# Kernel tuning notes

Hardware: AMD Instinct MI355X
Metric: run time of the kernel (lower is better)

Reference implementation:

```python
import jax, jax.numpy as jnp
import numpy as np

EPS = 1e-30
NEG = -1e30  # finite stand-in for -inf (safe under vjp, exp underflows to 0)


def _build_tree(L):
    """Perfect binary tree with L leaves (L power of 2) plus a unifurcating root.
    Node ids are level-contiguous (leaves first), which is a valid postorder-compatible
    numbering for the level-synchronous pruning loop."""
    depth = int(np.log2(L))
    total = 2 * L  # (2L-1) perfect-tree nodes + 1 unifurcating root
    children = np.full((total, 2), -1, dtype=np.int64)
    parents = np.full(total, -1, dtype=np.int64)
    levels = np.zeros(total, dtype=np.int64)
    offs = np.zeros(depth + 1, dtype=np.int64)
    for h in range(1, depth + 1):
        offs[h] = offs[h - 1] + (L >> (h - 1))
    for h in range(1, depth + 1):
        n = L >> h
        ids = offs[h] + np.arange(n)
        lkid = offs[h - 1] + 2 * np.arange(n)
        children[ids, 0] = lkid
        children[ids, 1] = lkid + 1
        parents[lkid] = ids
        parents[lkid + 1] = ids
        levels[ids] = h
    root = total - 1
    top = offs[depth]  # the single node at level `depth`
    children[root, 0] = top  # unifurcating root: right child = -1
    parents[top] = root
    levels[root] = depth + 1
    return children, parents, levels


def setup_inputs() -> dict:
    key = jax.random.key(0)
    S = 16
    L = 32768  # leaves -> N = 65536 nodes
    children, parents, levels = _build_tree(L)
    N = children.shape[0]
    postorder = np.arange(N, dtype=np.int64)
    k1, k2, k3, k4 = jax.random.split(key, 4)
    branch_lens = jax.random.uniform(k1, (N,), jnp.float32, 0.05, 0.5)
    branch_lens = branch_lens.at[N - 1].set(0.0)  # root edge has length 0
    # CTMC-style rate matrix: nonneg off-diagonals, rows sum to 0
    off = jax.random.uniform(k2, (S, S), jnp.float32, 0.1, 1.0) * (1.0 - jnp.eye(S, dtype=jnp.float32))
    Q = off - jnp.diag(off.sum(axis=1))
    growth_rates = jax.random.uniform(k3, (S,), jnp.float32, 0.5, 1.5)
    leaf_states = np.asarray(jax.random.randint(k4, (L,), 0, S))
    init_partials = np.full((N, S), NEG, dtype=np.float32)
    init_partials[np.arange(L), leaf_states] = 0.0  # leaf one-hots in log space
    return {
        "postorder": jnp.asarray(postorder),
        "children": jnp.asarray(children),
        "parents": jnp.asarray(parents),
        "branch_lens": branch_lens,
        "init_partials": jnp.asarray(init_partials),
        "Q": Q,
        "levels": jnp.asarray(levels),
        "growth_rates": growth_rates,
    }


def _log_prune(branch_lens, init_partials, Q, growth_rates, po, ch, lv):
    S = Q.shape[0]
    # rho == 1.0 path of FelsensteinPruner.log_prune
    rate = Q - jnp.diag(growth_rates)
    scaled = rate[None, :, :] * branch_lens[:, None, None]      # (N, S, S)
    trans = jax.vmap(jax.scipy.linalg.expm)(scaled)             # batched matrix_exp
    I = jnp.eye(S, dtype=Q.dtype)
    trans = jnp.where((branch_lens <= EPS)[:, None, None], I[None], trans)
    log_trans = jnp.log(jnp.clip(trans, EPS))
    log_growth = jnp.log(growth_rates)
    log_partials = init_partials
    max_level = int(lv.max())
    for lvl in range(1, max_level + 1):  # tree topology is static -> static level groups
        node_idxs = po[lv == lvl]
        left = ch[node_idxs, 0]
        right = ch[node_idxs, 1]
        # left_contrib[n, p] = logsumexp_c( log P_left[n, p, c] + L_left[n, c] )
        lc = jax.nn.logsumexp(log_trans[left] + log_partials[left][:, None, :], axis=2)
        valid = np.nonzero(right >= 0)[0]
        rc = jnp.zeros_like(lc)
        if valid.size > 0:
            rv = right[valid]
            rc_v = jax.nn.logsumexp(log_trans[rv] + log_partials[rv][:, None, :], axis=2)
            rc_v = rc_v + log_growth[None, :]  # growth_rates term on the right child
            rc = rc.at[valid].set(rc_v)
        log_partials = log_partials.at[node_idxs].set(lc + rc)
    root = int(po[lv == max_level][0])
    return log_partials[root]


def reference(postorder, children, parents, branch_lens, init_partials, Q, levels, growth_rates):
    po = np.asarray(postorder)
    ch = np.asarray(children)
    lv = np.asarray(levels)
    return _log_prune(branch_lens, init_partials, Q, growth_rates, po, ch, lv)
```

## Files before the change

kernel.cpp:

```cpp
#include <hip/hip_runtime.h>
#include <math.h>

#define KORD 10
#define NC   (KORD + 1)
#define NTOT 65536
#define MAGIC 0x5A17C0DEu
#define NB   256
#define CB0  240

typedef float f32x2 __attribute__((ext_vector_type(2)));

static constexpr int WS_U7  = 0;
static constexpr int WS_S7  = 4096;
static constexpr int WS_U11 = 4352;
static constexpr int WS_S11 = 4608;
static constexpr int WS_F1  = 4624;
static constexpr int WS_F2  = 4880;


template <int CTRL>
__device__ __forceinline__ float qperm_add(float x) {
  const int xi = __builtin_bit_cast(int, x);
  const int yi = __builtin_amdgcn_mov_dpp(xi, CTRL, 0xF, 0xF, true);
  return x + __builtin_bit_cast(float, yi);
}

__device__ __forceinline__ float horner_dot(const f32x2* c01, const f32x2* c23,
                                            float tv, float4 uu) {
  const f32x2 t2 = {tv, tv};
  f32x2 a01 = c01[KORD], a23 = c23[KORD];
  #pragma unroll
  for (int k = KORD - 1; k >= 0; --k) {
    a01 = __builtin_elementwise_fma(a01, t2, c01[k]);
    a23 = __builtin_elementwise_fma(a23, t2, c23[k]);
  }
  const f32x2 u01 = {uu.x, uu.y}, u23 = {uu.z, uu.w};
  f32x2 mm = a01 * u01;
  mm = __builtin_elementwise_fma(a23, u23, mm);
  float yy = mm.x + mm.y;
  yy = qperm_add<0xB1>(yy);
  yy = qperm_add<0x4E>(yy);
  return yy;
}

__device__ __forceinline__ int tree_sweep(
    float* ubuf, float* sbuf, const float* blB,
    const f32x2* c01, const f32x2* c23, float sigma, float gp,
    int IN, int depth, int t)
{
  const int lane = t & 63;
  const int wid = t >> 6;
  const int p = (lane >> 2) & 15;
  const int q = lane & 3;
  int off_in = 0, bloff = 0;
  for (int ll = 1; ll <= depth; ++ll) {
    const int cnt = IN >> ll;
    const int off_out = off_in + (IN >> (ll - 1));
    for (int n = wid; n < cnt; n += 8) {
      const int cl = 2 * n, cr = cl + 1;
      const float tl = blB[bloff + cl];
      const float tr = blB[bloff + cr];
      const float4 uL = *(const float4*)&ubuf[(off_in + cl) * 16 + q * 4];
      const float4 uR = *(const float4*)&ubuf[(off_in + cr) * 16 + q * 4];
      const float yl = horner_dot(c01, c23, tl, uL);
      const float yr = horner_dot(c01, c23, tr, uR);
      const float val = yl * yr * gp;
      const float mx = __shfl(val, 28 + q, 64);
      const float un = val * __builtin_amdgcn_rcpf(mx);
      if (q == 0) ubuf[(off_out + n) * 16 + p] = un;
      if (lane == 0)
        sbuf[off_out + n] = sbuf[off_in + cl] + sbuf[off_in + cr] +
                            sigma * (tl + tr) + __logf(mx);
    }
    bloff += IN >> (ll - 1);
    off_in = off_out;
    __syncthreads();
  }
  return off_in;
}

__device__ __forceinline__ void stage_bl(float* blB, const float* bl,
                                         int grp, int IN, int depth,
                                         int level_in, int tt) {
  int loff = 0;
  for (int ll = 1; ll <= depth; ++ll) {
    const int cnt_c = IN >> (ll - 1);
    const int gl = level_in + ll - 1;
    const int cbase = (gl == 0) ? 0 : (NTOT - (NTOT >> gl));
    if (tt < cnt_c) blB[loff + tt] = bl[cbase + grp * cnt_c + tt];
    loff += cnt_c;
  }
}

__device__ __forceinline__ void poll_reset(unsigned int* f) {
  while (__hip_atomic_load(f, __ATOMIC_RELAXED, __HIP_MEMORY_SCOPE_AGENT)
         != MAGIC)
    __builtin_amdgcn_s_sleep(1);
  __hip_atomic_store(f, 0u, __ATOMIC_RELAXED, __HIP_MEMORY_SCOPE_AGENT);
}

__device__ __forceinline__ float row_dot16(const float4* row, const float* col) {
  const float4 r0 = row[0], r1 = row[1], r2 = row[2], r3 = row[3];
  float s = r0.x * col[0];
  s = fmaf(r0.y, col[1], s);  s = fmaf(r0.z, col[2], s);
  s = fmaf(r0.w, col[3], s);  s = fmaf(r1.x, col[4], s);
  s = fmaf(r1.y, col[5], s);  s = fmaf(r1.z, col[6], s);
  s = fmaf(r1.w, col[7], s);  s = fmaf(r2.x, col[8], s);
  s = fmaf(r2.y, col[9], s);  s = fmaf(r2.z, col[10], s);
  s = fmaf(r2.w, col[11], s); s = fmaf(r3.x, col[12], s);
  s = fmaf(r3.y, col[13], s); s = fmaf(r3.z, col[14], s);
  s = fmaf(r3.w, col[15], s);
  return s;
}

__global__ __launch_bounds__(512) void k_all(
    const float* __restrict__ bl, const float* __restrict__ init_p,
    const float* __restrict__ Q, const float* __restrict__ g,
    float* __restrict__ ws, float* __restrict__ out)
{
  __shared__ __align__(16) float Bs[256];
  __shared__ __align__(16) float BsT[256];
  __shared__ __align__(16) float B2T[256];
  __shared__ __align__(16) float Cs[NC * 256];
  __shared__ __align__(16) float ubuf[255 * 16];
  __shared__ float sbuf[255];
  __shared__ float blB[254];
  __shared__ float sdiag[16];
  __shared__ float s_sig;

  const int t = threadIdx.x, b = blockIdx.x;
  const int lane = t & 63, wid = t >> 6;
  const int p = (lane >> 2) & 15, q = lane & 3;
  const int i = (t & 255) >> 4, j = t & 15;
  const int tt = t - 256;
  unsigned int* f1 = (unsigned int*)(ws + WS_F1);
  unsigned int* f2 = (unsigned int*)(ws + WS_F2);

  float4 leafv = ((const float4*)init_p)[b * 512 + t];
  float blr[7];
  if (t >= 256) {
    int cnt = 128, base = 0;
    #pragma unroll
    for (int ll = 1; ll <= 7; ++ll) {
      if (tt < cnt) blr[ll - 1] = bl[base + b * cnt + tt];
      base = NTOT - (NTOT >> ll);
      cnt >>= 1;
    }
  }

  float a = 0.0f;
  if (t < 256) {
    a = Q[t] - ((i == j) ? g[i] : 0.0f);
    if (i == j) sdiag[i] = a;
  }
  __syncthreads();
  if (t == 0) {
    float m = sdiag[0];
    for (int r = 1; r < 16; ++r) m = fminf(m, sdiag[r]);
    s_sig = m;
  }
  __syncthreads();
  const float sigma = s_sig;
  if (t < 256) {
    const float bv = a - ((i == j) ? sigma : 0.0f);
    Bs[t] = bv;
    BsT[j * 16 + i] = bv;
    Cs[t] = (i == j) ? 1.0f : 0.0f;
    Cs[256 + t] = bv;
  }
  __syncthreads();
  if (t < 256) {
    float bcol[16];
    #pragma unroll
    for (int c = 0; c < 4; ++c)
      *(float4*)&bcol[c * 4] = *(const float4*)&BsT[j * 16 + c * 4];
    const float s = row_dot16((const float4*)&Bs[i * 16], bcol);
    B2T[j * 16 + i] = s;
  }
  __syncthreads();
  float b2col[16];
  #pragma unroll
  for (int c = 0; c < 4; ++c)
    *(float4*)&b2col[c * 4] = *(const float4*)&B2T[j * 16 + c * 4];
  #pragma unroll
  for (int m = 0; m < 5; ++m) {
    if (t < 256) {
      const float s = row_dot16((const float4*)&Cs[(2 * m) * 256 + i * 16], b2col);
      Cs[(2 * m + 2) * 256 + t] = s * (1.0f / (float)((2 * m + 1) * (2 * m + 2)));
    } else if (m < 4) {
      const float s = row_dot16((const float4*)&Cs[(2 * m + 1) * 256 + i * 16], b2col);
      Cs[(2 * m + 3) * 256 + tt] =
          s * (1.0f / (float)((2 * m + 2) * (2 * m + 3)));
    }
    __syncthreads();
  }
  f32x2 c01[NC], c23[NC];
  #pragma unroll
  for (int k = 0; k <= KORD; ++k) {
    const float4 v = *(const float4*)&Cs[k * 256 + p * 16 + q * 4];
    c01[k] = f32x2{v.x, v.y};
    c23[k] = f32x2{v.z, v.w};
  }
  const float gp = g[p];

  {
    float4 v = leafv;
    v.x = (v.x > -0.5f) ? 1.0f : 0.0f;
    v.y = (v.y > -0.5f) ? 1.0f : 0.0f;
    v.z = (v.z > -0.5f) ? 1.0f : 0.0f;
    v.w = (v.w > -0.5f) ? 1.0f : 0.0f;
    ((float4*)ubuf)[t] = v;
  }
  if (t < 128) sbuf[t] = 0.0f;
  if (t >= 256) {
    int loff = 0, cnt = 128;
    #pragma unroll
    for (int ll = 1; ll <= 7; ++ll) {
      if (tt < cnt) blB[loff + tt] = blr[ll - 1];
      loff += cnt;
      cnt >>= 1;
    }
  }
  __syncthreads();

  {
    const int off = tree_sweep(ubuf, sbuf, blB, c01, c23, sigma, gp, 128, 7, t);
    if (t < 16)
      __hip_atomic_store(&ws[WS_U7 + b * 16 + t], ubuf[off * 16 + t],
                         __ATOMIC_RELAXED, __HIP_MEMORY_SCOPE_AGENT);
    if (t == 16)
      __hip_atomic_store(&ws[WS_S7 + b], sbuf[off],
                         __ATOMIC_RELAXED, __HIP_MEMORY_SCOPE_AGENT);
    asm volatile("s_waitcnt vmcnt(0)" ::: "memory");
    if (t == 0)
      __hip_atomic_store(&f1[b], MAGIC,
                         __ATOMIC_RELAXED, __HIP_MEMORY_SCOPE_AGENT);
  }
  if (b < CB0) return;
  const int c = b - CB0;

  if (t < 16) poll_reset(&f1[c * 16 + t]);
  __syncthreads();
  if (t < 256)
    ubuf[t] = __hip_atomic_load(&ws[WS_U7 + c * 256 + t], __ATOMIC_RELAXED,
                                __HIP_MEMORY_SCOPE_AGENT);
  if (t < 16)
    sbuf[t] = __hip_atomic_load(&ws[WS_S7 + c * 16 + t], __ATOMIC_RELAXED,
                                __HIP_MEMORY_SCOPE_AGENT);
  if (t >= 256) stage_bl(blB, bl, c, 16, 4, 7, tt);
  __syncthreads();
  {
    const int off = tree_sweep(ubuf, sbuf, blB, c01, c23, sigma, gp, 16, 4, t);
    if (t < 16)
      __hip_atomic_store(&ws[WS_U11 + c * 16 + t], ubuf[off * 16 + t],
                         __ATOMIC_RELAXED, __HIP_MEMORY_SCOPE_AGENT);
    if (t == 16)
      __hip_atomic_store(&ws[WS_S11 + c], sbuf[off],
                         __ATOMIC_RELAXED, __HIP_MEMORY_SCOPE_AGENT);
    asm volatile("s_waitcnt vmcnt(0)" ::: "memory");
    if (t == 0)
      __hip_atomic_store(&f2[c], MAGIC,
                         __ATOMIC_RELAXED, __HIP_MEMORY_SCOPE_AGENT);
  }
  if (b != NB - 1) return;

  if (t < 16) poll_reset(&f2[t]);
  __syncthreads();
  if (t < 256)
    ubuf[t] = __hip_atomic_load(&ws[WS_U11 + t], __ATOMIC_RELAXED,
                                __HIP_MEMORY_SCOPE_AGENT);
  if (t < 16)
    sbuf[t] = __hip_atomic_load(&ws[WS_S11 + t], __ATOMIC_RELAXED,
                                __HIP_MEMORY_SCOPE_AGENT);
  if (t >= 256) stage_bl(blB, bl, 0, 16, 4, 11, tt);
  __syncthreads();
  {
    const int off = tree_sweep(ubuf, sbuf, blB, c01, c23, sigma, gp, 16, 4, t);
    if (wid == 0) {
      const float tr = bl[NTOT - 2];
      const float4 u = *(const float4*)&ubuf[off * 16 + q * 4];
      const float y = horner_dot(c01, c23, tr, u);
      if (q == 0) out[p] = logf(y) + sbuf[off] + sigma * tr;
    }
  }
}

extern "C" void kernel_launch(void* const* d_in, const int* in_sizes, int n_in,
                              void* d_out, int out_size, void* d_ws, size_t ws_size,
                              hipStream_t stream) {
  const float* bl     = (const float*)d_in[3];
  const float* init_p = (const float*)d_in[4];
  const float* Q      = (const float*)d_in[5];
  const float* growth = (const float*)d_in[7];
  float* ws  = (float*)d_ws;
  float* out = (float*)d_out;

  k_all<<<NB, 512, 0, stream>>>(bl, init_p, Q, growth, ws, out);
}
```

Measured before the change: 23.84 us.

## Fuse pairs of tree levels per wave to halve block barriers

Each wave now processes a grandparent task: it evaluates four grandchildren, forms two intermediate parents through a per-wave LDS scratch buffer, then computes the grandparent, so two tree levels share one __syncthreads. This cuts the number of block-wide barriers in each sweep roughly in half. The cost is an intra-wave LDS round trip and less parallelism on levels with few nodes. Intermediate-level normalization is skipped, so the unnormalized products could lose range.

Result: faster. 20.74 us, median of 2 (-13.0%).

```diff
diff --git a/kernel.cpp b/kernel.cpp
--- a/kernel.cpp
+++ b/kernel.cpp
@@ -43,8 +43,8 @@
   return yy;
 }
 
-__device__ __forceinline__ int tree_sweep(
-    float* ubuf, float* sbuf, const float* blB,
+__device__ __forceinline__ int tree_sweep_fused(
+    float* ubuf, float* sbuf, const float* blB, float* pv,
     const f32x2* c01, const f32x2* c23, float sigma, float gp,
     int IN, int depth, int t)
 {
@@ -52,29 +52,72 @@
   const int wid = t >> 6;
   const int p = (lane >> 2) & 15;
   const int q = lane & 3;
-  int off_in = 0, bloff = 0;
-  for (int ll = 1; ll <= depth; ++ll) {
-    const int cnt = IN >> ll;
-    const int off_out = off_in + (IN >> (ll - 1));
+  int off_in = 0, bloff = 0, cur = IN, rem = depth;
+
+  while (rem >= 2) {
+    const int tasks = cur >> 2;
+    const int off_out = off_in + cur + (cur >> 1);
+    const int bloff_p = bloff + cur;
+    for (int n = wid; n < tasks; n += 8) {
+      const float4 tc = *(const float4*)&blB[bloff + 4 * n];
+      const float2 tp = *(const float2*)&blB[bloff_p + 2 * n];
+      const float4 u0 = *(const float4*)&ubuf[(off_in + 4 * n + 0) * 16 + q * 4];
+      const float4 u1 = *(const float4*)&ubuf[(off_in + 4 * n + 1) * 16 + q * 4];
+      const float4 u2 = *(const float4*)&ubuf[(off_in + 4 * n + 2) * 16 + q * 4];
+      const float4 u3 = *(const float4*)&ubuf[(off_in + 4 * n + 3) * 16 + q * 4];
+      const float y0 = horner_dot(c01, c23, tc.x, u0);
+      const float y1 = horner_dot(c01, c23, tc.y, u1);
+      const float y2 = horner_dot(c01, c23, tc.z, u2);
+      const float y3 = horner_dot(c01, c23, tc.w, u3);
+      const float v0 = y0 * y1 * gp;
+      const float v1 = y2 * y3 * gp;
+      if (q == 0) {
+        pv[wid * 32 + p] = v0;
+        pv[wid * 32 + 16 + p] = v1;
+      }
+      asm volatile("s_waitcnt lgkmcnt(0)" ::: "memory");
+      const float4 w0 = *(const float4*)&pv[wid * 32 + q * 4];
+      const float4 w1 = *(const float4*)&pv[wid * 32 + 16 + q * 4];
+      const float z0 = horner_dot(c01, c23, tp.x, w0);
+      const float z1 = horner_dot(c01, c23, tp.y, w1);
+      const float zz = z0 * z1 * gp;
+      const float mx = __shfl(zz, 28 + q, 64);
+      const float un = zz * __builtin_amdgcn_rcpf(mx);
+      if (q == 0) ubuf[(off_out + n) * 16 + p] = un;
+      if (lane == 0) {
+        const float4 sc = *(const float4*)&sbuf[off_in + 4 * n];
+        sbuf[off_out + n] = sc.x + sc.y + sc.z + sc.w +
+                            sigma * (tc.x + tc.y + tc.z + tc.w + tp.x + tp.y) +
+                            __logf(mx);
+      }
+    }
+    __syncthreads();
+    bloff += cur + (cur >> 1);
+    off_in = off_out;
+    cur >>= 2;
+    rem -= 2;
+  }
+
+  if (rem == 1) {
+    const int cnt = cur >> 1;
+    const int off_out = off_in + cur;
     for (int n = wid; n < cnt; n += 8) {
-      const int cl = 2 * n, cr = cl + 1;
-      const float tl = blB[bloff + cl];
-      const float tr = blB[bloff + cr];
-      const float4 uL = *(const float4*)&ubuf[(off_in + cl) * 16 + q * 4];
-      const float4 uR = *(const float4*)&ubuf[(off_in + cr) * 16 + q * 4];
-      const float yl = horner_dot(c01, c23, tl, uL);
-      const float yr = horner_dot(c01, c23, tr, uR);
+      const float2 tl2 = *(const float2*)&blB[bloff + 2 * n];
+      const float4 uL = *(const float4*)&ubuf[(off_in + 2 * n) * 16 + q * 4];
+      const float4 uR = *(const float4*)&ubuf[(off_in + 2 * n + 1) * 16 + q * 4];
+      const float yl = horner_dot(c01, c23, tl2.x, uL);
+      const float yr = horner_dot(c01, c23, tl2.y, uR);
       const float val = yl * yr * gp;
       const float mx = __shfl(val, 28 + q, 64);
       const float un = val * __builtin_amdgcn_rcpf(mx);
       if (q == 0) ubuf[(off_out + n) * 16 + p] = un;
-      if (lane == 0)
-        sbuf[off_out + n] = sbuf[off_in + cl] + sbuf[off_in + cr] +
-                            sigma * (tl + tr) + __logf(mx);
-    }
-    bloff += IN >> (ll - 1);
+      if (lane == 0) {
+        const float2 sc = *(const float2*)&sbuf[off_in + 2 * n];
+        sbuf[off_out + n] = sc.x + sc.y + sigma * (tl2.x + tl2.y) + __logf(mx);
+      }
+    }
+    __syncthreads();
     off_in = off_out;
-    __syncthreads();
   }
   return off_in;
 }
@@ -123,8 +166,9 @@
   __shared__ __align__(16) float B2T[256];
   __shared__ __align__(16) float Cs[NC * 256];
   __shared__ __align__(16) float ubuf[255 * 16];
-  __shared__ float sbuf[255];
-  __shared__ float blB[254];
+  __shared__ __align__(16) float sbuf[256];
+  __shared__ __align__(16) float blB[256];
+  __shared__ __align__(16) float pv[8 * 32];
   __shared__ float sdiag[16];
   __shared__ float s_sig;
 
@@ -224,7 +268,8 @@
   __syncthreads();
 
   {
-    const int off = tree_sweep(ubuf, sbuf, blB, c01, c23, sigma, gp, 128, 7, t);
+    const int off = tree_sweep_fused(ubuf, sbuf, blB, pv, c01, c23, sigma, gp,
+                                     128, 7, t);
     if (t < 16)
       __hip_atomic_store(&ws[WS_U7 + b * 16 + t], ubuf[off * 16 + t],
                          __ATOMIC_RELAXED, __HIP_MEMORY_SCOPE_AGENT);
@@ -250,7 +295,8 @@
   if (t >= 256) stage_bl(blB, bl, c, 16, 4, 7, tt);
   __syncthreads();
   {
-    const int off = tree_sweep(ubuf, sbuf, blB, c01, c23, sigma, gp, 16, 4, t);
+    const int off = tree_sweep_fused(ubuf, sbuf, blB, pv, c01, c23, sigma, gp,
+                                     16, 4, t);
     if (t < 16)
       __hip_atomic_store(&ws[WS_U11 + c * 16 + t], ubuf[off * 16 + t],
                          __ATOMIC_RELAXED, __HIP_MEMORY_SCOPE_AGENT);
@@ -275,7 +321,8 @@
   if (t >= 256) stage_bl(blB, bl, 0, 16, 4, 11, tt);
   __syncthreads();
   {
-    const int off = tree_sweep(ubuf, sbuf, blB, c01, c23, sigma, gp, 16, 4, t);
+    const int off = tree_sweep_fused(ubuf, sbuf, blB, pv, c01, c23, sigma, gp,
+                                     16, 4, t);
     if (wid == 0) {
       const float tr = bl[NTOT - 2];
       const float4 u = *(const float4*)&ubuf[off * 16 + q * 4];
```
